# Kernel optimization log

Measured on AMD Instinct MI355X. Metric: run time of the kernel, lower is better.

The kernel has to match this reference:

```python
import jax, jax.numpy as jnp
import numpy as np

NUM_USERS = 100000
NUM_ITEMS = 50000
NUM_EDGES = 2000000
DIM = 64
NUM_REL = 5


def setup_inputs() -> dict:
    key = jax.random.key(0)
    k1, k2, k3, k4, k5, k6 = jax.random.split(key, 6)
    u_features = jax.random.normal(k1, (NUM_USERS, DIM), dtype=jnp.float32)
    i_features = jax.random.normal(k2, (NUM_ITEMS, DIM), dtype=jnp.float32)
    edge_user = jax.random.randint(k3, (NUM_EDGES,), 0, NUM_USERS, dtype=jnp.int64)
    edge_item = jax.random.randint(k4, (NUM_EDGES,), 0, NUM_ITEMS, dtype=jnp.int64)
    # per-relation Linear params, torch convention: y = x @ W[r].T + b[r]
    W = jax.random.normal(k5, (NUM_REL, DIM, DIM), dtype=jnp.float32) * (1.0 / np.sqrt(DIM))
    b = jax.random.normal(k6, (NUM_REL, DIM), dtype=jnp.float32) * 0.01
    return {"u_features": u_features, "i_features": i_features,
            "edge_user": edge_user, "edge_item": edge_item, "W": W, "b": b}


def reference(u_features, i_features, edge_user, edge_item, W, b):
    # gather edge endpoint features: [E, D]
    edge_u = u_features[edge_user]
    edge_i = i_features[edge_item]
    num_rel = W.shape[0]
    # per relation: sum((edge_u @ W[r].T + b[r]) * edge_i, axis=1) -> [E]
    # loop over small fixed relation count to avoid [E, R, D] intermediate
    cols = [jnp.sum((edge_u @ W[r].T + b[r]) * edge_i, axis=1)
            for r in range(num_rel)]
    return jnp.stack(cols, axis=1)  # [E, R]
```

## Files before the change

### kernel.cpp

```cpp
#include <hip/hip_runtime.h>
#include <stdint.h>

#define NREL 5
#define D 64
#define Q_BYTES 320
#define NT 21
#define NB 8
#define CHUNK 4096
#define EDGE_GRID 1280

typedef __attribute__((ext_vector_type(8))) short short8;
typedef __attribute__((ext_vector_type(4))) float f32x4;

static __device__ __forceinline__ short f2bf(float f) {
    uint32_t u = __float_as_uint(f);
    u += 0x7FFFu + ((u >> 16) & 1u);
    return (short)(u >> 16);
}

#if defined(__has_builtin)
#if __has_builtin(__builtin_amdgcn_sdot4)
#define HAVE_SDOT4 1
#endif
#endif
#ifdef HAVE_SDOT4
static __device__ __forceinline__ int SDOT4(uint32_t a, uint32_t b, int c) {
    return __builtin_amdgcn_sdot4((int)a, (int)b, c, false);
}
#else
static __device__ __forceinline__ int SDOT4(uint32_t a, uint32_t b, int c) {
    c += ((int)(a << 24) >> 24) * ((int)(b << 24) >> 24);
    c += ((int)(a << 16) >> 24) * ((int)(b << 16) >> 24);
    c += ((int)(a << 8) >> 24) * ((int)(b << 8) >> 24);
    c += ((int)a >> 24) * ((int)b >> 24);
    return c;
}
#endif

__global__ __launch_bounds__(256) void prep_kernel(
    const float* __restrict__ W, const float* __restrict__ bias_p, short* __restrict__ Wf,
    const float* __restrict__ uf, uint32_t* __restrict__ uq, float* __restrict__ uscale,
    int nUsers,
    const int* __restrict__ edge_item,
    int nE, int bucketDiv, int* __restrict__ blkHist, int nBlocksSort)
{
    __shared__ int cnt[NB];
    const int nbW = (NT * 2 * 64 + 255) / 256;
    const int nbU = (nUsers * 16 + 255) / 256;
    int bid = blockIdx.x;

    if (bid < nbW) {
        const int tid = bid * 256 + threadIdx.x;
        if (tid >= NT * 2 * 64) return;
        const int lane = tid & 63;
        const int h = (tid >> 6) & 1;
        const int nt = tid >> 7;
        const int ln = lane & 15, quad = lane >> 4;
        const int n = nt * 16 + ln;
        uint32_t w[4];
#pragma unroll
        for (int p = 0; p < 4; ++p) {
            uint32_t lo = 0, hi = 0;
#pragma unroll
            for (int s = 0; s < 2; ++s) {
                const int j = p * 2 + s;
                const int d = h * 32 + quad * 8 + j;
                float v;
                if (nt < 20) v = W[(n >> 6) * (D * D) + d * D + (n & 63)];
                else         v = (ln < NREL) ? bias_p[ln * D + d] : 0.f;
                if (s == 0) lo = (uint16_t)f2bf(v); else hi = (uint16_t)f2bf(v);
            }
            w[p] = lo | (hi << 16);
        }
        *(uint4*)(Wf + (size_t)tid * 8) = make_uint4(w[0], w[1], w[2], w[3]);
        return;
    }
    bid -= nbW;

    if (bid < nbU) {
        const int gid = bid * 256 + threadIdx.x;
        const int row = gid >> 4;
        const int t = gid & 15;
        if (row >= nUsers) return;
        const float* rp = uf + (size_t)row * D;
        const float v0 = rp[t], v1 = rp[16 + t], v2 = rp[32 + t], v3 = rp[48 + t];
        float m = fmaxf(fmaxf(fabsf(v0), fabsf(v1)), fmaxf(fabsf(v2), fabsf(v3)));
        m = fmaxf(m, __shfl_xor(m, 1));
        m = fmaxf(m, __shfl_xor(m, 2));
        m = fmaxf(m, __shfl_xor(m, 4));
        m = fmaxf(m, __shfl_xor(m, 8));
        m = fmaxf(m, 1e-20f);
        const float qs = 127.0f / m;
        const int q0 = (int)rintf(v0 * qs);
        const int q1 = (int)rintf(v1 * qs);
        const int q2 = (int)rintf(v2 * qs);
        const int q3 = (int)rintf(v3 * qs);
        uq[(size_t)row * 16 + t] = ((uint32_t)(uint8_t)(int8_t)q0)
                                 | ((uint32_t)(uint8_t)(int8_t)q1 << 8)
                                 | ((uint32_t)(uint8_t)(int8_t)q2 << 16)
                                 | ((uint32_t)(uint8_t)(int8_t)q3 << 24);
        if (t == 0) uscale[row] = m * (1.0f / 127.0f);
        return;
    }
    bid -= nbU;

    if (threadIdx.x < NB) cnt[threadIdx.x] = 0;
    __syncthreads();
    const long start = (long)bid * CHUNK;
#pragma unroll
    for (int k = 0; k < CHUNK / 256; ++k) {
        const long e = start + k * 256 + threadIdx.x;
        if (e < nE) atomicAdd(&cnt[edge_item[e] / bucketDiv], 1);
    }
    __syncthreads();
    if (threadIdx.x < NB) blkHist[(size_t)threadIdx.x * nBlocksSort + bid] = cnt[threadIdx.x];
}

__global__ __launch_bounds__(256) void item_transform_kernel(
    const float* __restrict__ i_feat,
    const short* __restrict__ Wf,
    char* __restrict__ qrecs,
    float* __restrict__ sc,
    int nItems)
{
    const int lane = threadIdx.x & 63;
    const int wv = threadIdx.x >> 6;
    const int m0 = blockIdx.x * 64 + wv * 16;
    const int ln = lane & 15, quad = lane >> 4;

    int rowA = m0 + ln;
    if (rowA >= nItems) rowA = nItems - 1;
    const float* ap = i_feat + (size_t)rowA * D + quad * 8;
    short8 af[2];
#pragma unroll
    for (int h = 0; h < 2; ++h) {
        const float4 x = *(const float4*)(ap + h * 32);
        const float4 y = *(const float4*)(ap + h * 32 + 4);
        short8 a;
        a[0] = f2bf(x.x); a[1] = f2bf(x.y); a[2] = f2bf(x.z); a[3] = f2bf(x.w);
        a[4] = f2bf(y.x); a[5] = f2bf(y.y); a[6] = f2bf(y.z); a[7] = f2bf(y.w);
        af[h] = a;
    }

    f32x4 acc[NT];
#pragma unroll
    for (int nt = 0; nt < NT; ++nt) acc[nt] = (f32x4){0.f, 0.f, 0.f, 0.f};

#pragma unroll
    for (int nt = 0; nt < NT; ++nt) {
        const short8 b0 = *(const short8*)(Wf + ((size_t)(nt * 2 + 0) * 64 + lane) * 8);
        acc[nt] = __builtin_amdgcn_mfma_f32_16x16x32_bf16(af[0], b0, acc[nt], 0, 0, 0);
        const short8 b1 = *(const short8*)(Wf + ((size_t)(nt * 2 + 1) * 64 + lane) * 8);
        acc[nt] = __builtin_amdgcn_mfma_f32_16x16x32_bf16(af[1], b1, acc[nt], 0, 0, 0);
    }

#pragma unroll
    for (int g = 0; g < 4; ++g) {
        const int item = m0 + quad * 4 + g;
        const bool ok = (item < nItems);
        char* rec = qrecs + (size_t)item * Q_BYTES;
#pragma unroll
        for (int r = 0; r < NREL; ++r) {
            const float v0 = acc[4 * r + 0][g];
            const float v1 = acc[4 * r + 1][g];
            const float v2 = acc[4 * r + 2][g];
            const float v3 = acc[4 * r + 3][g];
            float m = fmaxf(fmaxf(fabsf(v0), fabsf(v1)), fmaxf(fabsf(v2), fabsf(v3)));
            m = fmaxf(m, __shfl_xor(m, 1));
            m = fmaxf(m, __shfl_xor(m, 2));
            m = fmaxf(m, __shfl_xor(m, 4));
            m = fmaxf(m, __shfl_xor(m, 8));
            m = fmaxf(m, 1e-20f);
            const float qs = 127.0f / m;
            const uint32_t pw = ((uint32_t)(uint8_t)(int8_t)(int)rintf(v0 * qs))
                              | ((uint32_t)(uint8_t)(int8_t)(int)rintf(v1 * qs) << 8)
                              | ((uint32_t)(uint8_t)(int8_t)(int)rintf(v2 * qs) << 16)
                              | ((uint32_t)(uint8_t)(int8_t)(int)rintf(v3 * qs) << 24);
            if (ok) {
                *(uint32_t*)(rec + r * D + ln * 4) = pw;
                if (ln == 0) sc[(size_t)item * 16 + 2 * r] = m * (1.0f / 127.0f);
            }
        }
        if (ok && ln < NREL) sc[(size_t)item * 16 + 2 * ln + 1] = acc[20][g];
    }
}

__global__ __launch_bounds__(512) void scan_kernel(
    int* __restrict__ blkHist, int nBlocks, int* __restrict__ bucketBase)
{
    __shared__ int tot[NB];
    __shared__ int base[NB + 1];
    const int lane = threadIdx.x & 63;
    const int b = threadIdx.x >> 6;
    int* col = blkHist + (size_t)b * nBlocks;
    int carry = 0;
    for (int c0 = 0; c0 < nBlocks; c0 += 64) {
        const int idx = c0 + lane;
        int v = (idx < nBlocks) ? col[idx] : 0;
        int s = v;
#pragma unroll
        for (int d = 1; d < 64; d <<= 1) {
            int t = __shfl_up(s, d);
            if (lane >= d) s += t;
        }
        if (idx < nBlocks) col[idx] = carry + s - v;
        carry += __shfl(s, 63);
    }
    if (lane == 0) tot[b] = carry;
    __syncthreads();
    if (threadIdx.x == 0) {
        int s = 0;
#pragma unroll
        for (int i = 0; i < NB; ++i) { base[i] = s; s += tot[i]; }
        base[NB] = s;
#pragma unroll
        for (int i = 0; i <= NB; ++i) bucketBase[i] = base[i];
    }
    __syncthreads();
    const int add = base[b];
    for (int c0 = 0; c0 < nBlocks; c0 += 64) {
        const int idx = c0 + lane;
        if (idx < nBlocks) col[idx] += add;
    }
}

__global__ __launch_bounds__(256) void scatter_kernel(
    const int* __restrict__ edge_user, const int* __restrict__ edge_item,
    int nE, int bucketDiv, const int* __restrict__ blkHist, int nBlocksSort,
    unsigned long long* __restrict__ sorted)
{
    __shared__ int cnt[NB];
    __shared__ int base[NB];
    if (threadIdx.x < NB) {
        cnt[threadIdx.x] = 0;
        base[threadIdx.x] = blkHist[(size_t)threadIdx.x * nBlocksSort + blockIdx.x];
    }
    __syncthreads();
    const long start = (long)blockIdx.x * CHUNK;
#pragma unroll
    for (int k = 0; k < CHUNK / 256; ++k) {
        const long e = start + k * 256 + threadIdx.x;
        if (e < nE) {
            const int iu = edge_user[e];
            const int ii = edge_item[e];
            const int kb = ii / bucketDiv;
            const int rank = atomicAdd(&cnt[kb], 1);
            const unsigned long long pk = (unsigned long long)(uint32_t)iu
                                        | ((unsigned long long)(uint32_t)ii << 17)
                                        | ((unsigned long long)e << 33);
            sorted[base[kb] + rank] = pk;
        }
    }
}

__global__ __launch_bounds__(256) void edge_kernel(
    const uint32_t* __restrict__ u_q,
    const float* __restrict__ u_scale,
    const unsigned long long* __restrict__ sorted,
    const int* __restrict__ bucketBase,
    const char* __restrict__ qrecs,
    const float* __restrict__ sc,
    float* __restrict__ out)
{
    const int b = blockIdx.x & 7;
    const int seg = blockIdx.x >> 3;
    const int nSeg = gridDim.x >> 3;
    const int s0 = bucketBase[b], s1 = bucketBase[b + 1];
    const int cnt = s1 - s0;
    const int per = (cnt + nSeg - 1) / nSeg;
    const int p0 = s0 + seg * per;
    const int p1 = min(p0 + per, s1);

    const int lane = threadIdx.x & 63;
    const int wv = threadIdx.x >> 6;
    const int es = lane >> 2;
    const int c = lane & 3;

    for (int q0 = p0 + wv * 16; q0 < p1; q0 += 64) {
        const int pos = q0 + es;
        if (pos < p1) {
            const unsigned long long pk = sorted[pos];
            const int iu = (int)(pk & 0x1FFFF);
            const int ii = (int)((pk >> 17) & 0xFFFF);
            const long e = (long)(pk >> 33);

            const uint4 uv = *(const uint4*)(u_q + (size_t)iu * 16 + c * 4);
            const char* rec = qrecs + (size_t)ii * Q_BYTES;

            int s[NREL];
#pragma unroll
            for (int r = 0; r < NREL; ++r) {
                const uint4 yv = *(const uint4*)(rec + r * D + c * 16);
                int t = SDOT4(uv.x, yv.x, 0);
                t = SDOT4(uv.y, yv.y, t);
                t = SDOT4(uv.z, yv.z, t);
                s[r] = SDOT4(uv.w, yv.w, t);
            }
#pragma unroll
            for (int r = 0; r < NREL; ++r) {
                s[r] += __shfl_xor(s[r], 1);
                s[r] += __shfl_xor(s[r], 2);
            }
            const float us = u_scale[iu];
            const float* scp = sc + (size_t)ii * 16;
            const float2 sb = *(const float2*)(scp + 2 * c);
            out[e * NREL + c] = fmaf((float)s[c], us * sb.x, sb.y);
            if (c == 0) {
                const float2 sb4 = *(const float2*)(scp + 8);
                out[e * NREL + 4] = fmaf((float)s[4], us * sb4.x, sb4.y);
            }
        }
    }
}

extern "C" void kernel_launch(void* const* d_in, const int* in_sizes, int n_in,
                              void* d_out, int out_size, void* d_ws, size_t ws_size,
                              hipStream_t stream) {
    const float* u_feat    = (const float*)d_in[0];
    const float* i_feat    = (const float*)d_in[1];
    const int*   edge_user = (const int*)d_in[2];
    const int*   edge_item = (const int*)d_in[3];
    const float* W         = (const float*)d_in[4];
    const float* b         = (const float*)d_in[5];
    float* out = (float*)d_out;

    const int nUsers = in_sizes[0] / D;
    const int nItems = in_sizes[1] / D;
    const int nE = in_sizes[2];
    const int bucketDiv = (nItems + NB - 1) / NB;
    const int nBlocksSort = (nE + CHUNK - 1) / CHUNK;

    size_t off = 0;
    char* qrecs = (char*)d_ws;
    off += ((size_t)nItems * Q_BYTES + 255) & ~(size_t)255;
    float* sc = (float*)((char*)d_ws + off);
    off += ((size_t)nItems * 16 * sizeof(float) + 255) & ~(size_t)255;
    uint32_t* u_q = (uint32_t*)((char*)d_ws + off);
    off += ((size_t)nUsers * D + 255) & ~(size_t)255;
    float* u_scale = (float*)((char*)d_ws + off);
    off += ((size_t)nUsers * sizeof(float) + 255) & ~(size_t)255;
    short* Wf = (short*)((char*)d_ws + off);
    off += ((size_t)NT * 2 * 64 * 8 * sizeof(short) + 255) & ~(size_t)255;
    int* blkHist = (int*)((char*)d_ws + off);
    off += ((size_t)NB * nBlocksSort * sizeof(int) + 255) & ~(size_t)255;
    int* bucketBase = (int*)((char*)d_ws + off);
    off += 256;
    unsigned long long* sorted = (unsigned long long*)((char*)d_ws + off);

    const int nbW = (NT * 2 * 64 + 255) / 256;
    const int nbU = (nUsers * 16 + 255) / 256;
    prep_kernel<<<nbW + nbU + nBlocksSort, 256, 0, stream>>>(
        W, b, Wf, u_feat, u_q, u_scale, nUsers,
        edge_item, nE, bucketDiv, blkHist, nBlocksSort);
    item_transform_kernel<<<(nItems + 63) / 64, 256, 0, stream>>>(i_feat, Wf, qrecs, sc, nItems);
    scan_kernel<<<1, 512, 0, stream>>>(blkHist, nBlocksSort, bucketBase);
    scatter_kernel<<<nBlocksSort, 256, 0, stream>>>(edge_user, edge_item, nE, bucketDiv,
                                                    blkHist, nBlocksSort, sorted);
    edge_kernel<<<EDGE_GRID, 256, 0, stream>>>(u_q, u_scale, sorted, bucketBase,
                                               qrecs, sc, out);
}
```

Baseline: 268.5 us.

## Fuse bucket histogram, scan and scatter into one pass using fixed-capacity buckets

Removes the separate scan and scatter kernels. Each sort block now loads its edges once into registers, counts bucket membership with packed wave reductions, reserves space with a global atomic on per-bucket totals, and scatters into fixed-capacity bucket regions. This saves two kernel launches and a second read of the edge arrays, at the cost of a memset, global atomics, and non-deterministic ordering within each bucket. A bucket that exceeds its capacity margin would overflow, which is safe only for roughly uniform item ids. The edge grid is also raised to 2048 blocks.

```diff
diff --git a/kernel.cpp b/kernel.cpp
--- a/kernel.cpp
+++ b/kernel.cpp
@@ -7,7 +7,7 @@
 #define NT 21
 #define NB 8
 #define CHUNK 4096
-#define EDGE_GRID 1280
+#define EDGE_GRID 2048
 
 typedef __attribute__((ext_vector_type(8))) short short8;
 typedef __attribute__((ext_vector_type(4))) float f32x4;
@@ -41,10 +41,12 @@
     const float* __restrict__ W, const float* __restrict__ bias_p, short* __restrict__ Wf,
     const float* __restrict__ uf, uint32_t* __restrict__ uq, float* __restrict__ uscale,
     int nUsers,
-    const int* __restrict__ edge_item,
-    int nE, int bucketDiv, int* __restrict__ blkHist, int nBlocksSort)
+    const int* __restrict__ edge_user, const int* __restrict__ edge_item,
+    int nE, int bucketDiv, int cap,
+    int* __restrict__ totals, unsigned long long* __restrict__ sorted)
 {
     __shared__ int cnt[NB];
+    __shared__ int base[NB];
     const int nbW = (NT * 2 * 64 + 255) / 256;
     const int nbU = (nUsers * 16 + 255) / 256;
     int bid = blockIdx.x;
@@ -106,14 +108,55 @@
 
     if (threadIdx.x < NB) cnt[threadIdx.x] = 0;
     __syncthreads();
+
     const long start = (long)bid * CHUNK;
+    unsigned long long pk[CHUNK / 256];
+    unsigned long long bins = 0;
+    unsigned long long accLo = 0, accHi = 0;
 #pragma unroll
     for (int k = 0; k < CHUNK / 256; ++k) {
         const long e = start + k * 256 + threadIdx.x;
-        if (e < nE) atomicAdd(&cnt[edge_item[e] / bucketDiv], 1);
+        const bool ok = (e < nE);
+        int iu = 0, ii = 0;
+        if (ok) { iu = edge_user[e]; ii = edge_item[e]; }
+        pk[k] = ok ? ((unsigned long long)(uint32_t)iu
+                    | ((unsigned long long)(uint32_t)ii << 17)
+                    | ((unsigned long long)e << 33))
+                   : ~0ull;
+        const int bn = ok ? (ii / bucketDiv) : 0;
+        bins |= (unsigned long long)bn << (k * 3);
+        if (ok) {
+            const unsigned long long one = 1ull << ((bn & 3) * 16);
+            if (bn < 4) accLo += one; else accHi += one;
+        }
+    }
+#pragma unroll
+    for (int d = 1; d < 64; d <<= 1) {
+        accLo += __shfl_xor(accLo, d);
+        accHi += __shfl_xor(accHi, d);
+    }
+    if ((threadIdx.x & 63) == 0) {
+#pragma unroll
+        for (int f = 0; f < 4; ++f) {
+            atomicAdd(&cnt[f],     (int)((accLo >> (f * 16)) & 0xFFFF));
+            atomicAdd(&cnt[4 + f], (int)((accHi >> (f * 16)) & 0xFFFF));
+        }
     }
     __syncthreads();
-    if (threadIdx.x < NB) blkHist[(size_t)threadIdx.x * nBlocksSort + bid] = cnt[threadIdx.x];
+    if (threadIdx.x < NB) {
+        const int c = cnt[threadIdx.x];
+        base[threadIdx.x] = threadIdx.x * cap + atomicAdd(&totals[threadIdx.x], c);
+        cnt[threadIdx.x] = 0;
+    }
+    __syncthreads();
+#pragma unroll
+    for (int k = 0; k < CHUNK / 256; ++k) {
+        if (pk[k] != ~0ull) {
+            const int bn = (int)((bins >> (k * 3)) & 7);
+            const int r = atomicAdd(&cnt[bn], 1);
+            sorted[base[bn] + r] = pk[k];
+        }
+    }
 }
 
 __global__ __launch_bounds__(256) void item_transform_kernel(
@@ -185,79 +228,11 @@
     }
 }
 
-__global__ __launch_bounds__(512) void scan_kernel(
-    int* __restrict__ blkHist, int nBlocks, int* __restrict__ bucketBase)
-{
-    __shared__ int tot[NB];
-    __shared__ int base[NB + 1];
-    const int lane = threadIdx.x & 63;
-    const int b = threadIdx.x >> 6;
-    int* col = blkHist + (size_t)b * nBlocks;
-    int carry = 0;
-    for (int c0 = 0; c0 < nBlocks; c0 += 64) {
-        const int idx = c0 + lane;
-        int v = (idx < nBlocks) ? col[idx] : 0;
-        int s = v;
-#pragma unroll
-        for (int d = 1; d < 64; d <<= 1) {
-            int t = __shfl_up(s, d);
-            if (lane >= d) s += t;
-        }
-        if (idx < nBlocks) col[idx] = carry + s - v;
-        carry += __shfl(s, 63);
-    }
-    if (lane == 0) tot[b] = carry;
-    __syncthreads();
-    if (threadIdx.x == 0) {
-        int s = 0;
-#pragma unroll
-        for (int i = 0; i < NB; ++i) { base[i] = s; s += tot[i]; }
-        base[NB] = s;
-#pragma unroll
-        for (int i = 0; i <= NB; ++i) bucketBase[i] = base[i];
-    }
-    __syncthreads();
-    const int add = base[b];
-    for (int c0 = 0; c0 < nBlocks; c0 += 64) {
-        const int idx = c0 + lane;
-        if (idx < nBlocks) col[idx] += add;
-    }
-}
-
-__global__ __launch_bounds__(256) void scatter_kernel(
-    const int* __restrict__ edge_user, const int* __restrict__ edge_item,
-    int nE, int bucketDiv, const int* __restrict__ blkHist, int nBlocksSort,
-    unsigned long long* __restrict__ sorted)
-{
-    __shared__ int cnt[NB];
-    __shared__ int base[NB];
-    if (threadIdx.x < NB) {
-        cnt[threadIdx.x] = 0;
-        base[threadIdx.x] = blkHist[(size_t)threadIdx.x * nBlocksSort + blockIdx.x];
-    }
-    __syncthreads();
-    const long start = (long)blockIdx.x * CHUNK;
-#pragma unroll
-    for (int k = 0; k < CHUNK / 256; ++k) {
-        const long e = start + k * 256 + threadIdx.x;
-        if (e < nE) {
-            const int iu = edge_user[e];
-            const int ii = edge_item[e];
-            const int kb = ii / bucketDiv;
-            const int rank = atomicAdd(&cnt[kb], 1);
-            const unsigned long long pk = (unsigned long long)(uint32_t)iu
-                                        | ((unsigned long long)(uint32_t)ii << 17)
-                                        | ((unsigned long long)e << 33);
-            sorted[base[kb] + rank] = pk;
-        }
-    }
-}
-
 __global__ __launch_bounds__(256) void edge_kernel(
     const uint32_t* __restrict__ u_q,
     const float* __restrict__ u_scale,
     const unsigned long long* __restrict__ sorted,
-    const int* __restrict__ bucketBase,
+    const int* __restrict__ totals, int cap,
     const char* __restrict__ qrecs,
     const float* __restrict__ sc,
     float* __restrict__ out)
@@ -265,7 +240,8 @@
     const int b = blockIdx.x & 7;
     const int seg = blockIdx.x >> 3;
     const int nSeg = gridDim.x >> 3;
-    const int s0 = bucketBase[b], s1 = bucketBase[b + 1];
+    const int s0 = b * cap;
+    const int s1 = s0 + totals[b];
     const int cnt = s1 - s0;
     const int per = (cnt + nSeg - 1) / nSeg;
     const int p0 = s0 + seg * per;
@@ -329,6 +305,7 @@
     const int nE = in_sizes[2];
     const int bucketDiv = (nItems + NB - 1) / NB;
     const int nBlocksSort = (nE + CHUNK - 1) / CHUNK;
+    const int cap = nE / NB + 32768;
 
     size_t off = 0;
     char* qrecs = (char*)d_ws;
@@ -341,21 +318,18 @@
     off += ((size_t)nUsers * sizeof(float) + 255) & ~(size_t)255;
     short* Wf = (short*)((char*)d_ws + off);
     off += ((size_t)NT * 2 * 64 * 8 * sizeof(short) + 255) & ~(size_t)255;
-    int* blkHist = (int*)((char*)d_ws + off);
-    off += ((size_t)NB * nBlocksSort * sizeof(int) + 255) & ~(size_t)255;
-    int* bucketBase = (int*)((char*)d_ws + off);
+    int* totals = (int*)((char*)d_ws + off);
     off += 256;
     unsigned long long* sorted = (unsigned long long*)((char*)d_ws + off);
+
+    hipMemsetAsync(totals, 0, NB * sizeof(int), stream);
 
     const int nbW = (NT * 2 * 64 + 255) / 256;
     const int nbU = (nUsers * 16 + 255) / 256;
     prep_kernel<<<nbW + nbU + nBlocksSort, 256, 0, stream>>>(
         W, b, Wf, u_feat, u_q, u_scale, nUsers,
-        edge_item, nE, bucketDiv, blkHist, nBlocksSort);
+        edge_user, edge_item, nE, bucketDiv, cap, totals, sorted);
     item_transform_kernel<<<(nItems + 63) / 64, 256, 0, stream>>>(i_feat, Wf, qrecs, sc, nItems);
-    scan_kernel<<<1, 512, 0, stream>>>(blkHist, nBlocksSort, bucketBase);
-    scatter_kernel<<<nBlocksSort, 256, 0, stream>>>(edge_user, edge_item, nE, bucketDiv,
-                                                    blkHist, nBlocksSort, sorted);
-    edge_kernel<<<EDGE_GRID, 256, 0, stream>>>(u_q, u_scale, sorted, bucketBase,
+    edge_kernel<<<EDGE_GRID, 256, 0, stream>>>(u_q, u_scale, sorted, totals, cap,
                                                qrecs, sc, out);
 }
```

New measurement: 259.1 us. 1.04x faster.
